# Performance work log

Measured on AMD Instinct MI355X. Metric: run time of the kernel, lower is better.

## Reference

```python
import jax, jax.numpy as jnp
import numpy as np

B, T, D = 64, 512, 128          # batch, time, input_dim
S = 16                           # num_sessions
P, STRIDE = 3, 1                 # patch size / stride
H = 512                          # hidden_size
HORIZONS = (1, 5, 10)
K = len(HORIZONS)
TOK = D * P                      # token_dim = 384
EPS = 1e-6


def setup_inputs() -> dict:
    key = jax.random.key(0)
    ks = jax.random.split(key, 16)
    s = 0.02
    return {
        "x": jax.random.normal(ks[0], (B, T, D), jnp.float32),
        "session_idx": jax.random.randint(ks[1], (B,), 0, S),
        # per-session affine (expert) params
        "sess_W": jax.random.normal(ks[2], (S, D, D), jnp.float32) * s,
        "sess_b": jax.random.normal(ks[3], (S, D), jnp.float32) * s,
        # projection token_dim -> hidden
        "proj_W": jax.random.normal(ks[4], (H, TOK), jnp.float32) * s,
        "proj_b": jax.random.normal(ks[5], (H,), jnp.float32) * s,
        "rms_scale": jnp.ones((H,), jnp.float32),
        # single-layer GRU params (PyTorch layout: [3H, in], gate order r,z,n)
        "gru_Wih": jax.random.normal(ks[6], (3 * H, H), jnp.float32) * s,
        "gru_Whh": jax.random.normal(ks[7], (3 * H, H), jnp.float32) * s,
        "gru_bih": jax.random.normal(ks[8], (3 * H,), jnp.float32) * s,
        "gru_bhh": jax.random.normal(ks[9], (3 * H,), jnp.float32) * s,
        # future heads (K horizons): Linear(H,H) -> GELU -> Linear(H,TOK)
        "head_W1": jax.random.normal(ks[10], (K, H, H), jnp.float32) * s,
        "head_b1": jax.random.normal(ks[11], (K, H), jnp.float32) * s,
        "head_W2": jax.random.normal(ks[12], (K, TOK, H), jnp.float32) * s,
        "head_b2": jax.random.normal(ks[13], (K, TOK), jnp.float32) * s,
    }


def _forward(x, session_idx, sess_W, sess_b, proj_W, proj_b, rms_scale,
             gru_Wih, gru_Whh, gru_bih, gru_bhh,
             head_W1, head_b1, head_W2, head_b2):
    # --- per-sample session affine (expert gather + batched GEMM) ---
    W = sess_W[session_idx]                      # [B, D, D]
    b = sess_b[session_idx]                      # [B, D]
    aligned = jnp.einsum('btd,bed->bte', x, W) + b[:, None, :]  # y = x @ W.T + b

    # --- patch unfold along time; torch unfold gives [N, D, P] -> flatten (d,p) ---
    N = (T - P) // STRIDE + 1
    idx = jnp.arange(N)[:, None] * STRIDE + jnp.arange(P)[None, :]  # [N, P]
    win = aligned[:, idx, :]                     # [B, N, P, D]
    tokens = jnp.transpose(win, (0, 1, 3, 2)).reshape(B, N, TOK)    # [B, N, D*P]

    # --- projection + RMSNorm ---
    h = tokens @ proj_W.T + proj_b               # [B, N, H]
    rms = jnp.sqrt(jnp.mean(h * h, axis=-1, keepdims=True) + EPS)
    h = h / rms * rms_scale

    # --- GRU (PyTorch gate order r, z, n) via lax.scan over time ---
    gx = h @ gru_Wih.T + gru_bih                 # [B, N, 3H], precomputed input gates
    gx_t = jnp.transpose(gx, (1, 0, 2))          # [N, B, 3H]

    def step(hprev, g):
        gh = hprev @ gru_Whh.T + gru_bhh         # [B, 3H]
        r = jax.nn.sigmoid(g[:, :H] + gh[:, :H])
        z = jax.nn.sigmoid(g[:, H:2 * H] + gh[:, H:2 * H])
        n = jnp.tanh(g[:, 2 * H:] + r * gh[:, 2 * H:])
        hn = (1.0 - z) * n + z * hprev
        return hn, hn

    h0 = jnp.zeros((B, H), h.dtype)
    _, hs = jax.lax.scan(step, h0, gx_t)         # [N, B, H]
    hidden = jnp.transpose(hs, (1, 0, 2))        # [B, N, H]

    # --- multi-head future MLPs (stacked over K horizons) ---
    a = jnp.einsum('bnh,kfh->kbnf', hidden, head_W1) + head_b1[:, None, None, :]
    a = jax.nn.gelu(a, approximate=False)        # torch nn.GELU default = exact
    preds = jnp.einsum('kbnf,ktf->kbnt', a, head_W2) + head_b2[:, None, None, :]
    return preds, tokens                          # preds: [K, B, N, TOK]


def reference(x, session_idx, sess_W, sess_b, proj_W, proj_b, rms_scale,
              gru_Wih, gru_Whh, gru_bih, gru_bhh,
              head_W1, head_b1, head_W2, head_b2):
    return _forward(x, session_idx, sess_W, sess_b, proj_W, proj_b, rms_scale,
                    gru_Wih, gru_Whh, gru_bih, gru_bhh,
                    head_W1, head_b1, head_W2, head_b2)
```

## Files before the change

### kernel.cpp

```cpp
#include <hip/hip_runtime.h>
#include <hip/hip_bf16.h>
#include <math.h>

typedef __hip_bfloat16 bf16;
typedef __attribute__((ext_vector_type(8))) short short8;
typedef __attribute__((ext_vector_type(4))) short short4v;
typedef __attribute__((ext_vector_type(4))) float f32x4;

#define B_    64
#define T_    512
#define D_    128
#define N_    510
#define H_    512
#define TOK_  384
#define PRED1_ 12533760L
#define TOKOFF_ 37601280L

#define O_XBF  0UL
#define O_SWB  8388608UL
#define O_PW   8912896UL
#define O_WIH  9306112UL
#define O_WHH  10878976UL
#define O_W1   12451840UL
#define O_W2   14024704UL
#define O_TOK  15204352UL
#define O_HBF  40271872UL
#define O_HID  73695232UL
#define O_ABF  107118592UL
#define O_GX   140541952UL

#define HID_BYTES 33423360UL

__global__ void k_f2b(const float* __restrict__ s, bf16* __restrict__ d, int n4) {
  int i = blockIdx.x * 256 + threadIdx.x;
  if (i < n4) {
    float4 v = ((const float4*)s)[i];
    union { short4v sv; bf16 h[4]; } u;
    u.h[0] = __float2bfloat16(v.x); u.h[1] = __float2bfloat16(v.y);
    u.h[2] = __float2bfloat16(v.z); u.h[3] = __float2bfloat16(v.w);
    ((short4v*)d)[i] = u.sv;
  }
}

enum { EPI_F32 = 0, EPI_BF16 = 1, EPI_GELU = 2, EPI_TOK = 3, EPI_F32R = 4 };
#define SLDA 40

template <int EPI>
__global__ __launch_bounds__(256, 2) void k_gemm(
    const bf16* __restrict__ A, const bf16* __restrict__ W,
    const float* __restrict__ bias, void* __restrict__ C,
    int K, int ldc, long zA, long zW, long zB, long zC,
    const int* __restrict__ sidx, float* __restrict__ tokf, bf16* __restrict__ tokb)
{
  const int tid = threadIdx.x;
  const int bm = blockIdx.x, bn = blockIdx.y, z = blockIdx.z;
  const int wsel = (EPI == EPI_TOK) ? sidx[z] : z;
  const int lane = tid & 63, wave = tid >> 6;
  const int wm = (wave & 1) << 6, wn = (wave >> 1) << 6;
  const int r16 = lane & 15, quad = lane >> 4;

  __shared__ bf16 sA[128 * SLDA];
  __shared__ bf16 sB[128 * SLDA];

  const bf16* Ag = A + (long)z * zA + (long)bm * 128 * K;
  const bf16* Wg = W + (long)wsel * zW + (long)bn * 128 * K;

  f32x4 zf = {0.f, 0.f, 0.f, 0.f};
  f32x4 acc[4][4];
  for (int i = 0; i < 4; ++i) for (int j = 0; j < 4; ++j) acc[i][j] = zf;

  const int sr = tid >> 1, sc = (tid & 1) << 4;
  for (int k0 = 0; k0 < K; k0 += 32) {
    *(short8*)&sA[sr*SLDA + sc]     = *(const short8*)&Ag[(long)sr*K + k0 + sc];
    *(short8*)&sA[sr*SLDA + sc + 8] = *(const short8*)&Ag[(long)sr*K + k0 + sc + 8];
    *(short8*)&sB[sr*SLDA + sc]     = *(const short8*)&Wg[(long)sr*K + k0 + sc];
    *(short8*)&sB[sr*SLDA + sc + 8] = *(const short8*)&Wg[(long)sr*K + k0 + sc + 8];
    __syncthreads();
    short8 fa[4], fb[4];
    for (int i = 0; i < 4; ++i) fa[i] = *(const short8*)&sA[(wm + i*16 + r16)*SLDA + quad*8];
    for (int j = 0; j < 4; ++j) fb[j] = *(const short8*)&sB[(wn + j*16 + r16)*SLDA + quad*8];
    for (int i = 0; i < 4; ++i)
      for (int j = 0; j < 4; ++j)
        acc[i][j] = __builtin_amdgcn_mfma_f32_16x16x32_bf16(fa[i], fb[j], acc[i][j], 0, 0, 0);
    __syncthreads();
  }

  const float* bz = bias + (long)wsel * zB + bn * 128;
  for (int i = 0; i < 4; ++i) {
    for (int j = 0; j < 4; ++j) {
      const int colL = wn + j*16 + r16;
      const float bv = bz[colL];
      for (int r = 0; r < 4; ++r) {
        float v = acc[i][j][r] + bv;
        const long grow = (long)bm*128 + wm + i*16 + quad*4 + r;
        const long gcol = (long)bn*128 + colL;
        if (EPI == EPI_F32) {
          ((float*)C)[(long)z*zC + grow*ldc + gcol] = v;
        } else if (EPI == EPI_BF16) {
          ((bf16*)C)[(long)z*zC + grow*ldc + gcol] = __float2bfloat16(v);
        } else if (EPI == EPI_GELU) {
          v = 0.5f * v * (1.0f + erff(v * 0.70710678118654752f));
          ((bf16*)C)[(long)z*zC + grow*ldc + gcol] = __float2bfloat16(v);
        } else if (EPI == EPI_F32R) {
          const long rb = grow & 63, rn = grow >> 6;
          ((float*)C)[(rb*510 + rn)*ldc + gcol] = v;
        } else {
          for (int p = 0; p < 3; ++p) {
            long n = grow - p;
            if (n >= 0 && n < N_) {
              tokf[((long)z*N_ + n)*TOK_ + gcol*3 + p] = v;
              tokb[((long)n*B_ + z)*TOK_ + gcol*3 + p] = __float2bfloat16(v);
            }
          }
        }
      }
    }
  }
}

__global__ __launch_bounds__(256) void k_rms(const float* __restrict__ hpre,
                                             const float* __restrict__ scale,
                                             bf16* __restrict__ hbf)
{
  const int wave = threadIdx.x >> 6, lane = threadIdx.x & 63;
  const long row = (long)blockIdx.x * 4 + wave;
  const float* p = hpre + row * 512 + lane * 8;
  float4 v0 = *(const float4*)p;
  float4 v1 = *(const float4*)(p + 4);
  float ss = v0.x*v0.x + v0.y*v0.y + v0.z*v0.z + v0.w*v0.w
           + v1.x*v1.x + v1.y*v1.y + v1.z*v1.z + v1.w*v1.w;
  for (int m = 32; m >= 1; m >>= 1) ss += __shfl_xor(ss, m, 64);
  const float inv = 1.0f / sqrtf(ss * (1.0f/512.0f) + 1e-6f);
  const float* sc = scale + lane * 8;
  union { short8 sv; bf16 h[8]; } u;
  u.h[0] = __float2bfloat16(v0.x*inv*sc[0]); u.h[1] = __float2bfloat16(v0.y*inv*sc[1]);
  u.h[2] = __float2bfloat16(v0.z*inv*sc[2]); u.h[3] = __float2bfloat16(v0.w*inv*sc[3]);
  u.h[4] = __float2bfloat16(v1.x*inv*sc[4]); u.h[5] = __float2bfloat16(v1.y*inv*sc[5]);
  u.h[6] = __float2bfloat16(v1.z*inv*sc[6]); u.h[7] = __float2bfloat16(v1.w*inv*sc[7]);
  *(short8*)(hbf + row * 512 + lane * 8) = u.sv;
}

#define KP 520

#define GL2LDS(g, l) __builtin_amdgcn_global_load_lds( \
    (const __attribute__((address_space(1))) void*)(g), \
    (__attribute__((address_space(3))) void*)(l), 16, 0, 16)

__global__ __launch_bounds__(64, 1) void k_gru(
    const bf16* __restrict__ gx,
    const bf16* __restrict__ Whh,
    const float* __restrict__ bhh,
    bf16* __restrict__ hidden)
{
  const int lane = threadIdx.x & 63;
  const int c16  = lane & 15, quad = lane >> 4;
  const int pw   = blockIdx.x & 31;
  const int gb   = blockIdx.x >> 5;
  const int hwv  = pw * 16;
  const int b0   = gb * 8;

  __shared__ bf16 wlds[16 * 3 * 64 * 8];
  __shared__ bf16 hp[8 * KP];

  for (int g3 = 0; g3 < 3; ++g3)
    for (int kt = 0; kt < 16; ++kt)
      *(short8*)&wlds[((kt*3 + g3)*64 + lane)*8] =
          *(const short8*)&Whh[(long)(g3*512 + hwv + c16)*512 + kt*32 + quad*8];
  const float bhr = bhh[       hwv + c16];
  const float bhz = bhh[ 512 + hwv + c16];
  const float bhn = bhh[1024 + hwv + c16];
  __syncthreads();

  const int brv = (quad & 1) * 4;

  float gr[4], gz[4], gn[4];
  float hcur[4] = {0.f, 0.f, 0.f, 0.f};
  {
    const bf16* gxs = gx + (long)b0 * 1536 + hwv + c16;
#pragma unroll
    for (int i2 = 0; i2 < 4; ++i2) {
      const long ro = (long)(brv + i2) * 1536;
      gr[i2] = __bfloat162float(gxs[ro]);
      gz[i2] = __bfloat162float(gxs[ro + 512]);
      gn[i2] = __bfloat162float(gxs[ro + 1024]);
    }
  }

  for (int s = 0; s < 510; ++s) {
    f32x4 ar = {0.f,0.f,0.f,0.f}, az = {0.f,0.f,0.f,0.f}, an = {0.f,0.f,0.f,0.f};

    if (s > 0) {
      union AU { unsigned u[4]; short8 s8; } au[16];
      const bf16* src = hidden + ((long)(s-1)*64 + b0)*512 + lane*8;
      while (true) {
#pragma unroll
        for (int b = 0; b < 8; ++b) GL2LDS(src + b*512, &hp[b*KP]);
        asm volatile("s_waitcnt vmcnt(0)" ::: "memory");
        unsigned mx = 0u;
#pragma unroll
        for (int kt = 0; kt < 16; ++kt) {
          au[kt].s8 = *(const short8*)&hp[(c16 & 7)*KP + kt*32 + quad*8];
          unsigned m01 = au[kt].u[0] > au[kt].u[1] ? au[kt].u[0] : au[kt].u[1];
          unsigned m23 = au[kt].u[2] > au[kt].u[3] ? au[kt].u[2] : au[kt].u[3];
          unsigned m = m01 > m23 ? m01 : m23;
          mx = mx > m ? mx : m;
        }
        if (__all(mx != 0xFFFFFFFFu)) break;
      }

#pragma unroll
      for (int kt = 0; kt < 16; ++kt) {
        short8 fr = *(const short8*)&wlds[((kt*3 + 0)*64 + lane)*8];
        short8 fz = *(const short8*)&wlds[((kt*3 + 1)*64 + lane)*8];
        short8 fn = *(const short8*)&wlds[((kt*3 + 2)*64 + lane)*8];
        ar = __builtin_amdgcn_mfma_f32_16x16x32_bf16(au[kt].s8, fr, ar, 0, 0, 0);
        az = __builtin_amdgcn_mfma_f32_16x16x32_bf16(au[kt].s8, fz, az, 0, 0, 0);
        an = __builtin_amdgcn_mfma_f32_16x16x32_bf16(au[kt].s8, fn, an, 0, 0, 0);
      }
    }

    if (quad < 2) {
#pragma unroll
      for (int i2 = 0; i2 < 4; ++i2) {
        const float r  = 1.0f / (1.0f + expf(-(gr[i2] + ar[i2] + bhr)));
        const float z  = 1.0f / (1.0f + expf(-(gz[i2] + az[i2] + bhz)));
        const float nn = tanhf(gn[i2] + r * (an[i2] + bhn));
        const float hn = (1.0f - z)*nn + z*hcur[i2];
        union { bf16 h; unsigned short u; } cb; cb.h = __float2bfloat16(hn);
        hcur[i2] = __bfloat162float(cb.h);
        unsigned mine = cb.u;
        unsigned part = (unsigned)__shfl_xor((int)mine, 1, 64);
        if (!(c16 & 1)) {
          unsigned w = (part << 16) | mine;
          __hip_atomic_store((unsigned*)(hidden + ((long)s*64 + b0 + brv + i2)*512 + hwv + c16),
                             w, __ATOMIC_RELAXED, __HIP_MEMORY_SCOPE_AGENT);
        }
      }
    }
    if (s < 509) {
      asm volatile("" ::: "memory");
      const bf16* gxs = gx + ((long)(s+1)*64 + b0)*1536 + hwv + c16;
#pragma unroll
      for (int i2 = 0; i2 < 4; ++i2) {
        const long ro = (long)(brv + i2) * 1536;
        gr[i2] = __bfloat162float(gxs[ro]);
        gz[i2] = __bfloat162float(gxs[ro + 512]);
        gn[i2] = __bfloat162float(gxs[ro + 1024]);
      }
    }
  }
}

extern "C" void kernel_launch(void* const* d_in, const int* in_sizes, int n_in,
                              void* d_out, int out_size, void* d_ws, size_t ws_size,
                              hipStream_t stream)
{
  const float* x    = (const float*)d_in[0];
  const int*   sidx = (const int*)d_in[1];
  const float* sW   = (const float*)d_in[2];
  const float* sb   = (const float*)d_in[3];
  const float* pW   = (const float*)d_in[4];
  const float* pb   = (const float*)d_in[5];
  const float* rsc  = (const float*)d_in[6];
  const float* wih  = (const float*)d_in[7];
  const float* whh  = (const float*)d_in[8];
  const float* bih  = (const float*)d_in[9];
  const float* bhh  = (const float*)d_in[10];
  const float* w1   = (const float*)d_in[11];
  const float* b1   = (const float*)d_in[12];
  const float* w2   = (const float*)d_in[13];
  const float* b2   = (const float*)d_in[14];
  char* ws = (char*)d_ws;
  float* out = (float*)d_out;

  bf16* xbf   = (bf16*)(ws + O_XBF);
  bf16* swbf  = (bf16*)(ws + O_SWB);
  bf16* pwbf  = (bf16*)(ws + O_PW);
  bf16* wihbf = (bf16*)(ws + O_WIH);
  bf16* whhbf = (bf16*)(ws + O_WHH);
  bf16* w1bf  = (bf16*)(ws + O_W1);
  bf16* w2bf  = (bf16*)(ws + O_W2);
  bf16* tokbf = (bf16*)(ws + O_TOK);
  bf16* hbf   = (bf16*)(ws + O_HBF);
  bf16* hidbf = (bf16*)(ws + O_HID);
  bf16* abf   = (bf16*)(ws + O_ABF);
  float* hpre = (float*)(ws + O_GX);
  bf16* gxbf  = (bf16*)(ws + O_GX);

  hipMemsetAsync(ws + O_HID, 0xFF, HID_BYTES, stream);

  auto cvt = [&](const float* s, bf16* dp, long n) {
    int n4 = (int)(n >> 2);
    k_f2b<<<dim3((n4 + 255) / 256), dim3(256), 0, stream>>>(s, dp, n4);
  };
  cvt(x,   xbf,   (long)B_*T_*D_);
  cvt(sW,  swbf,  16L*128*128);
  cvt(pW,  pwbf,  512L*384);
  cvt(wih, wihbf, 1536L*512);
  cvt(whh, whhbf, 1536L*512);
  cvt(w1,  w1bf,  3L*512*512);
  cvt(w2,  w2bf,  3L*384*512);

  k_gemm<EPI_TOK><<<dim3(4, 1, 64), dim3(256), 0, stream>>>(
      xbf, swbf, sb, nullptr, 128, 0,
      (long)T_*D_, 128L*128, 128L, 0L, sidx, out + TOKOFF_, tokbf);

  k_gemm<EPI_F32><<<dim3(255, 4, 1), dim3(256), 0, stream>>>(
      tokbf, pwbf, pb, hpre, 384, 512, 0, 0, 0, 0, nullptr, nullptr, nullptr);

  k_rms<<<dim3(8160), dim3(256), 0, stream>>>(hpre, rsc, hbf);

  k_gemm<EPI_BF16><<<dim3(255, 12, 1), dim3(256), 0, stream>>>(
      hbf, wihbf, bih, gxbf, 512, 1536, 0, 0, 0, 0, nullptr, nullptr, nullptr);

  k_gru<<<dim3(256), dim3(64), 0, stream>>>(gxbf, whhbf, bhh, hidbf);

  for (int k = 0; k < 3; ++k) {
    k_gemm<EPI_GELU><<<dim3(255, 4, 1), dim3(256), 0, stream>>>(
        hidbf, w1bf + (long)k*512*512, b1 + (long)k*512, abf,
        512, 512, 0, 0, 0, 0, nullptr, nullptr, nullptr);
    k_gemm<EPI_F32R><<<dim3(255, 3, 1), dim3(256), 0, stream>>>(
        abf, w2bf + (long)k*384*512, b2 + (long)k*384, out + (long)k*PRED1_,
        512, 384, 0, 0, 0, 0, nullptr, nullptr, nullptr);
  }
}
```

Baseline: 2.115 ms.

## Interleave two batch groups per GRU block with prefetched hidden-state loads

Each GRU workgroup now processes two 8-row batch groups (A and B) in alternation, and the grid shrinks from 256 to 128 blocks. After a group finishes a step, its LDS buffer is overwritten with a sentinel and the next step's hidden-state load is issued straight away. That load then completes while the other group computes, instead of being issued and waited on at the top of the loop. The aim is to hide inter-block polling and global-load latency on the recurrent critical path. The cost is halved parallelism and serialised work per block, and the sentinel-based readiness check depends on LDS write and load ordering.

```diff
diff --git a/kernel.cpp b/kernel.cpp
--- a/kernel.cpp
+++ b/kernel.cpp
@@ -146,6 +146,81 @@
     (const __attribute__((address_space(1))) void*)(g), \
     (__attribute__((address_space(3))) void*)(l), 16, 0, 16)
 
+#define GRU_PHASE(HP, B0, GR, GZ, GN, HC)                                        \
+  {                                                                              \
+    f32x4 ar = {0.f,0.f,0.f,0.f}, az = {0.f,0.f,0.f,0.f}, an = {0.f,0.f,0.f,0.f};\
+    if (s > 0) {                                                                 \
+      union AU { unsigned u[4]; short8 s8; } au[16];                             \
+      asm volatile("s_waitcnt vmcnt(24)" ::: "memory");                          \
+      while (true) {                                                             \
+        unsigned mx = 0u;                                                        \
+        _Pragma("unroll")                                                        \
+        for (int kt = 0; kt < 16; ++kt) {                                        \
+          au[kt].s8 = *(const short8*)&HP[(c16 & 7)*KP + kt*32 + quad*8];        \
+          unsigned m01 = au[kt].u[0] > au[kt].u[1] ? au[kt].u[0] : au[kt].u[1];  \
+          unsigned m23 = au[kt].u[2] > au[kt].u[3] ? au[kt].u[2] : au[kt].u[3];  \
+          unsigned m = m01 > m23 ? m01 : m23;                                    \
+          mx = mx > m ? mx : m;                                                  \
+        }                                                                        \
+        if (__all(mx != 0xFFFFFFFFu)) break;                                     \
+        const bf16* rsrc = hidden + ((long)(s-1)*64 + (B0))*512 + lane*8;        \
+        _Pragma("unroll")                                                        \
+        for (int b = 0; b < 8; ++b) GL2LDS(rsrc + b*512, &HP[b*KP]);             \
+        asm volatile("s_waitcnt vmcnt(0)" ::: "memory");                         \
+      }                                                                          \
+      _Pragma("unroll")                                                          \
+      for (int kt = 0; kt < 16; ++kt) {                                          \
+        short8 fr = *(const short8*)&wlds[((kt*3 + 0)*64 + lane)*8];             \
+        short8 fz = *(const short8*)&wlds[((kt*3 + 1)*64 + lane)*8];             \
+        short8 fn = *(const short8*)&wlds[((kt*3 + 2)*64 + lane)*8];             \
+        ar = __builtin_amdgcn_mfma_f32_16x16x32_bf16(au[kt].s8, fr, ar, 0, 0, 0);\
+        az = __builtin_amdgcn_mfma_f32_16x16x32_bf16(au[kt].s8, fz, az, 0, 0, 0);\
+        an = __builtin_amdgcn_mfma_f32_16x16x32_bf16(au[kt].s8, fn, an, 0, 0, 0);\
+      }                                                                          \
+    }                                                                            \
+    if (quad < 2) {                                                              \
+      _Pragma("unroll")                                                          \
+      for (int i2 = 0; i2 < 4; ++i2) {                                           \
+        const float r  = 1.0f / (1.0f + expf(-(GR[i2] + ar[i2] + bhr)));         \
+        const float z  = 1.0f / (1.0f + expf(-(GZ[i2] + az[i2] + bhz)));         \
+        const float nn = tanhf(GN[i2] + r * (an[i2] + bhn));                     \
+        const float hn = (1.0f - z)*nn + z*HC[i2];                               \
+        union { bf16 h; unsigned short u; } cb; cb.h = __float2bfloat16(hn);     \
+        HC[i2] = __bfloat162float(cb.h);                                         \
+        unsigned mine = cb.u;                                                    \
+        unsigned part = (unsigned)__shfl_xor((int)mine, 1, 64);                  \
+        if (!(c16 & 1)) {                                                        \
+          unsigned w = (part << 16) | mine;                                      \
+          __hip_atomic_store(                                                    \
+              (unsigned*)(hidden + ((long)s*64 + (B0) + brv + i2)*512 + hwv + c16),\
+              w, __ATOMIC_RELAXED, __HIP_MEMORY_SCOPE_AGENT);                    \
+        }                                                                        \
+      }                                                                          \
+    }                                                                            \
+    if (s < 509) {                                                               \
+          \
+      asm volatile("s_waitcnt lgkmcnt(0)" ::: "memory");                         \
+      _Pragma("unroll")                                                          \
+      for (int b = 0; b < 8; ++b) *(short8*)&HP[b*KP + lane*8] = sentv;          \
+      asm volatile("s_waitcnt lgkmcnt(0)" ::: "memory");                         \
+                \
+      const bf16* gxs = gx + ((long)(s+1)*64 + (B0))*1536 + hwv + c16;           \
+      _Pragma("unroll")                                                          \
+      for (int i2 = 0; i2 < 4; ++i2) {                                           \
+        const long ro = (long)(brv + i2) * 1536;                                 \
+        GR[i2] = __bfloat162float(gxs[ro]);                                      \
+        GZ[i2] = __bfloat162float(gxs[ro + 512]);                                \
+        GN[i2] = __bfloat162float(gxs[ro + 1024]);                               \
+      }                                                                          \
+      asm volatile("" ::: "memory");                                             \
+              \
+      const bf16* dsrc = hidden + ((long)s*64 + (B0))*512 + lane*8;              \
+      _Pragma("unroll")                                                          \
+      for (int b = 0; b < 8; ++b) GL2LDS(dsrc + b*512, &HP[b*KP]);               \
+      asm volatile("" ::: "memory");                                             \
+    }                                                                            \
+  }
+
 __global__ __launch_bounds__(64, 1) void k_gru(
     const bf16* __restrict__ gx,
     const bf16* __restrict__ Whh,
@@ -155,12 +230,14 @@
   const int lane = threadIdx.x & 63;
   const int c16  = lane & 15, quad = lane >> 4;
   const int pw   = blockIdx.x & 31;
-  const int gb   = blockIdx.x >> 5;
+  const int pr   = blockIdx.x >> 5;
   const int hwv  = pw * 16;
-  const int b0   = gb * 8;
+  const int bA   = pr * 16;
+  const int bB   = pr * 16 + 8;
 
   __shared__ bf16 wlds[16 * 3 * 64 * 8];
-  __shared__ bf16 hp[8 * KP];
+  __shared__ bf16 hpA[8 * KP];
+  __shared__ bf16 hpB[8 * KP];
 
   for (int g3 = 0; g3 < 3; ++g3)
     for (int kt = 0; kt < 16; ++kt)
@@ -171,83 +248,32 @@
   const float bhn = bhh[1024 + hwv + c16];
   __syncthreads();
 
+  union SU { unsigned u[4]; short8 s8; } su_;
+  su_.u[0] = su_.u[1] = su_.u[2] = su_.u[3] = 0xFFFFFFFFu;
+  const short8 sentv = su_.s8;
+
   const int brv = (quad & 1) * 4;
 
-  float gr[4], gz[4], gn[4];
-  float hcur[4] = {0.f, 0.f, 0.f, 0.f};
+  float grA[4], gzA[4], gnA[4], grB[4], gzB[4], gnB[4];
+  float hcA[4] = {0.f,0.f,0.f,0.f}, hcB[4] = {0.f,0.f,0.f,0.f};
   {
-    const bf16* gxs = gx + (long)b0 * 1536 + hwv + c16;
+    const bf16* ga = gx + (long)bA * 1536 + hwv + c16;
+    const bf16* gb = gx + (long)bB * 1536 + hwv + c16;
 #pragma unroll
     for (int i2 = 0; i2 < 4; ++i2) {
       const long ro = (long)(brv + i2) * 1536;
-      gr[i2] = __bfloat162float(gxs[ro]);
-      gz[i2] = __bfloat162float(gxs[ro + 512]);
-      gn[i2] = __bfloat162float(gxs[ro + 1024]);
+      grA[i2] = __bfloat162float(ga[ro]);
+      gzA[i2] = __bfloat162float(ga[ro + 512]);
+      gnA[i2] = __bfloat162float(ga[ro + 1024]);
+      grB[i2] = __bfloat162float(gb[ro]);
+      gzB[i2] = __bfloat162float(gb[ro + 512]);
+      gnB[i2] = __bfloat162float(gb[ro + 1024]);
     }
   }
 
   for (int s = 0; s < 510; ++s) {
-    f32x4 ar = {0.f,0.f,0.f,0.f}, az = {0.f,0.f,0.f,0.f}, an = {0.f,0.f,0.f,0.f};
-
-    if (s > 0) {
-      union AU { unsigned u[4]; short8 s8; } au[16];
-      const bf16* src = hidden + ((long)(s-1)*64 + b0)*512 + lane*8;
-      while (true) {
-#pragma unroll
-        for (int b = 0; b < 8; ++b) GL2LDS(src + b*512, &hp[b*KP]);
-        asm volatile("s_waitcnt vmcnt(0)" ::: "memory");
-        unsigned mx = 0u;
-#pragma unroll
-        for (int kt = 0; kt < 16; ++kt) {
-          au[kt].s8 = *(const short8*)&hp[(c16 & 7)*KP + kt*32 + quad*8];
-          unsigned m01 = au[kt].u[0] > au[kt].u[1] ? au[kt].u[0] : au[kt].u[1];
-          unsigned m23 = au[kt].u[2] > au[kt].u[3] ? au[kt].u[2] : au[kt].u[3];
-          unsigned m = m01 > m23 ? m01 : m23;
-          mx = mx > m ? mx : m;
-        }
-        if (__all(mx != 0xFFFFFFFFu)) break;
-      }
-
-#pragma unroll
-      for (int kt = 0; kt < 16; ++kt) {
-        short8 fr = *(const short8*)&wlds[((kt*3 + 0)*64 + lane)*8];
-        short8 fz = *(const short8*)&wlds[((kt*3 + 1)*64 + lane)*8];
-        short8 fn = *(const short8*)&wlds[((kt*3 + 2)*64 + lane)*8];
-        ar = __builtin_amdgcn_mfma_f32_16x16x32_bf16(au[kt].s8, fr, ar, 0, 0, 0);
-        az = __builtin_amdgcn_mfma_f32_16x16x32_bf16(au[kt].s8, fz, az, 0, 0, 0);
-        an = __builtin_amdgcn_mfma_f32_16x16x32_bf16(au[kt].s8, fn, an, 0, 0, 0);
-      }
-    }
-
-    if (quad < 2) {
-#pragma unroll
-      for (int i2 = 0; i2 < 4; ++i2) {
-        const float r  = 1.0f / (1.0f + expf(-(gr[i2] + ar[i2] + bhr)));
-        const float z  = 1.0f / (1.0f + expf(-(gz[i2] + az[i2] + bhz)));
-        const float nn = tanhf(gn[i2] + r * (an[i2] + bhn));
-        const float hn = (1.0f - z)*nn + z*hcur[i2];
-        union { bf16 h; unsigned short u; } cb; cb.h = __float2bfloat16(hn);
-        hcur[i2] = __bfloat162float(cb.h);
-        unsigned mine = cb.u;
-        unsigned part = (unsigned)__shfl_xor((int)mine, 1, 64);
-        if (!(c16 & 1)) {
-          unsigned w = (part << 16) | mine;
-          __hip_atomic_store((unsigned*)(hidden + ((long)s*64 + b0 + brv + i2)*512 + hwv + c16),
-                             w, __ATOMIC_RELAXED, __HIP_MEMORY_SCOPE_AGENT);
-        }
-      }
-    }
-    if (s < 509) {
-      asm volatile("" ::: "memory");
-      const bf16* gxs = gx + ((long)(s+1)*64 + b0)*1536 + hwv + c16;
-#pragma unroll
-      for (int i2 = 0; i2 < 4; ++i2) {
-        const long ro = (long)(brv + i2) * 1536;
-        gr[i2] = __bfloat162float(gxs[ro]);
-        gz[i2] = __bfloat162float(gxs[ro + 512]);
-        gn[i2] = __bfloat162float(gxs[ro + 1024]);
-      }
-    }
+    GRU_PHASE(hpA, bA, grA, gzA, gnA, hcA);
+    GRU_PHASE(hpB, bB, grB, gzB, gnB, hcB);
   }
 }
 
@@ -313,7 +339,7 @@
   k_gemm<EPI_BF16><<<dim3(255, 12, 1), dim3(256), 0, stream>>>(
       hbf, wihbf, bih, gxbf, 512, 1536, 0, 0, 0, 0, nullptr, nullptr, nullptr);
 
-  k_gru<<<dim3(256), dim3(64), 0, stream>>>(gxbf, whhbf, bhh, hidbf);
+  k_gru<<<dim3(128), dim3(64), 0, stream>>>(gxbf, whhbf, bhh, hidbf);
 
   for (int k = 0; k < 3; ++k) {
     k_gemm<EPI_GELU><<<dim3(255, 4, 1), dim3(256), 0, stream>>>(
```

Measured after the change: 3.607 ms. 70.6% more time.

## Split GRU recurrence gates across three waves per block with LDS exchange

Applied to the files above, without the earlier changes.

The persistent GRU kernel now runs three wavefronts per block, one per gate (r, z, n). Wave 0 polls for and loads the previous hidden state into LDS, and the other waves read it after a barrier. Each wave then does a third of the MFMA work, and r/z are passed through shared memory to wave 2, which computes the new state. The aim is to shorten the serial per-step latency by running the gate matmuls in parallel. The cost is two block barriers per step and an extra LDS round trip on the critical path.

```diff
diff --git a/kernel.cpp b/kernel.cpp
--- a/kernel.cpp
+++ b/kernel.cpp
@@ -146,13 +146,15 @@
     (const __attribute__((address_space(1))) void*)(g), \
     (__attribute__((address_space(3))) void*)(l), 16, 0, 16)
 
-__global__ __launch_bounds__(64, 1) void k_gru(
+__global__ __launch_bounds__(192, 1) void k_gru(
     const bf16* __restrict__ gx,
     const bf16* __restrict__ Whh,
     const float* __restrict__ bhh,
     bf16* __restrict__ hidden)
 {
-  const int lane = threadIdx.x & 63;
+  const int tid  = threadIdx.x;
+  const int wv   = tid / 64;
+  const int lane = tid & 63;
   const int c16  = lane & 15, quad = lane >> 4;
   const int pw   = blockIdx.x & 31;
   const int gb   = blockIdx.x >> 5;
@@ -161,36 +163,30 @@
 
   __shared__ bf16 wlds[16 * 3 * 64 * 8];
   __shared__ bf16 hp[8 * KP];
-
-  for (int g3 = 0; g3 < 3; ++g3)
-    for (int kt = 0; kt < 16; ++kt)
-      *(short8*)&wlds[((kt*3 + g3)*64 + lane)*8] =
-          *(const short8*)&Whh[(long)(g3*512 + hwv + c16)*512 + kt*32 + quad*8];
-  const float bhr = bhh[       hwv + c16];
-  const float bhz = bhh[ 512 + hwv + c16];
-  const float bhn = bhh[1024 + hwv + c16];
+  __shared__ float ex[2][8 * 16];
+
+  for (int kt = 0; kt < 16; ++kt)
+    *(short8*)&wlds[((kt*3 + wv)*64 + lane)*8] =
+        *(const short8*)&Whh[(long)(wv*512 + hwv + c16)*512 + kt*32 + quad*8];
+  const float bh = bhh[wv*512 + hwv + c16];
   __syncthreads();
 
   const int brv = (quad & 1) * 4;
 
-  float gr[4], gz[4], gn[4];
+  float gv[4];
   float hcur[4] = {0.f, 0.f, 0.f, 0.f};
   {
-    const bf16* gxs = gx + (long)b0 * 1536 + hwv + c16;
-#pragma unroll
-    for (int i2 = 0; i2 < 4; ++i2) {
-      const long ro = (long)(brv + i2) * 1536;
-      gr[i2] = __bfloat162float(gxs[ro]);
-      gz[i2] = __bfloat162float(gxs[ro + 512]);
-      gn[i2] = __bfloat162float(gxs[ro + 1024]);
-    }
+    const bf16* gxs = gx + (long)b0 * 1536 + wv*512 + hwv + c16;
+#pragma unroll
+    for (int i2 = 0; i2 < 4; ++i2)
+      gv[i2] = __bfloat162float(gxs[(long)(brv + i2) * 1536]);
   }
 
   for (int s = 0; s < 510; ++s) {
-    f32x4 ar = {0.f,0.f,0.f,0.f}, az = {0.f,0.f,0.f,0.f}, an = {0.f,0.f,0.f,0.f};
-
-    if (s > 0) {
-      union AU { unsigned u[4]; short8 s8; } au[16];
+    f32x4 acc = {0.f, 0.f, 0.f, 0.f};
+    union AU { unsigned u[4]; short8 s8; } au[16];
+
+    if (s > 0 && wv == 0) {
       const bf16* src = hidden + ((long)(s-1)*64 + b0)*512 + lane*8;
       while (true) {
 #pragma unroll
@@ -207,46 +203,58 @@
         }
         if (__all(mx != 0xFFFFFFFFu)) break;
       }
-
+    }
+    __syncthreads();
+
+    if (s > 0) {
+      if (wv != 0) {
+#pragma unroll
+        for (int kt = 0; kt < 16; ++kt)
+          au[kt].s8 = *(const short8*)&hp[(c16 & 7)*KP + kt*32 + quad*8];
+      }
 #pragma unroll
       for (int kt = 0; kt < 16; ++kt) {
-        short8 fr = *(const short8*)&wlds[((kt*3 + 0)*64 + lane)*8];
-        short8 fz = *(const short8*)&wlds[((kt*3 + 1)*64 + lane)*8];
-        short8 fn = *(const short8*)&wlds[((kt*3 + 2)*64 + lane)*8];
-        ar = __builtin_amdgcn_mfma_f32_16x16x32_bf16(au[kt].s8, fr, ar, 0, 0, 0);
-        az = __builtin_amdgcn_mfma_f32_16x16x32_bf16(au[kt].s8, fz, az, 0, 0, 0);
-        an = __builtin_amdgcn_mfma_f32_16x16x32_bf16(au[kt].s8, fn, an, 0, 0, 0);
-      }
-    }
-
-    if (quad < 2) {
+        short8 fb = *(const short8*)&wlds[((kt*3 + wv)*64 + lane)*8];
+        acc = __builtin_amdgcn_mfma_f32_16x16x32_bf16(au[kt].s8, fb, acc, 0, 0, 0);
+      }
+    }
+
+    if (wv < 2) {
+      if (quad < 2) {
+#pragma unroll
+        for (int i2 = 0; i2 < 4; ++i2)
+          ex[wv][(quad*4 + i2)*16 + c16] =
+              1.0f / (1.0f + expf(-(gv[i2] + acc[i2] + bh)));
+      }
+    }
+    asm volatile("s_waitcnt lgkmcnt(0)" ::: "memory");
+    __syncthreads();
+
+    if (wv == 2 && quad < 2) {
 #pragma unroll
       for (int i2 = 0; i2 < 4; ++i2) {
-        const float r  = 1.0f / (1.0f + expf(-(gr[i2] + ar[i2] + bhr)));
-        const float z  = 1.0f / (1.0f + expf(-(gz[i2] + az[i2] + bhz)));
-        const float nn = tanhf(gn[i2] + r * (an[i2] + bhn));
-        const float hn = (1.0f - z)*nn + z*hcur[i2];
+        const int br = brv + i2;
+        const float rr = ex[0][br*16 + c16];
+        const float zz = ex[1][br*16 + c16];
+        const float nn = tanhf(gv[i2] + rr * (acc[i2] + bh));
+        const float hn = (1.0f - zz)*nn + zz*hcur[i2];
         union { bf16 h; unsigned short u; } cb; cb.h = __float2bfloat16(hn);
         hcur[i2] = __bfloat162float(cb.h);
         unsigned mine = cb.u;
         unsigned part = (unsigned)__shfl_xor((int)mine, 1, 64);
         if (!(c16 & 1)) {
           unsigned w = (part << 16) | mine;
-          __hip_atomic_store((unsigned*)(hidden + ((long)s*64 + b0 + brv + i2)*512 + hwv + c16),
+          __hip_atomic_store((unsigned*)(hidden + ((long)s*64 + b0 + br)*512 + hwv + c16),
                              w, __ATOMIC_RELAXED, __HIP_MEMORY_SCOPE_AGENT);
         }
       }
     }
     if (s < 509) {
       asm volatile("" ::: "memory");
-      const bf16* gxs = gx + ((long)(s+1)*64 + b0)*1536 + hwv + c16;
-#pragma unroll
-      for (int i2 = 0; i2 < 4; ++i2) {
-        const long ro = (long)(brv + i2) * 1536;
-        gr[i2] = __bfloat162float(gxs[ro]);
-        gz[i2] = __bfloat162float(gxs[ro + 512]);
-        gn[i2] = __bfloat162float(gxs[ro + 1024]);
-      }
+      const bf16* gxs = gx + ((long)(s+1)*64 + b0)*1536 + wv*512 + hwv + c16;
+#pragma unroll
+      for (int i2 = 0; i2 < 4; ++i2)
+        gv[i2] = __bfloat162float(gxs[(long)(brv + i2) * 1536]);
     }
   }
 }
@@ -313,7 +321,7 @@
   k_gemm<EPI_BF16><<<dim3(255, 12, 1), dim3(256), 0, stream>>>(
       hbf, wihbf, bih, gxbf, 512, 1536, 0, 0, 0, 0, nullptr, nullptr, nullptr);
 
-  k_gru<<<dim3(256), dim3(64), 0, stream>>>(gxbf, whhbf, bhh, hidbf);
+  k_gru<<<dim3(256), dim3(192), 0, stream>>>(gxbf, whhbf, bhh, hidbf);
 
   for (int k = 0; k < 3; ++k) {
     k_gemm<EPI_GELU><<<dim3(255, 4, 1), dim3(256), 0, stream>>>(
```

After: 2.475 ms. 1.17x slower.
